# Optimization experiments

Hardware: AMD Instinct MI355X
Metric: run time of the kernel (lower is better)

## Reference

```python
import jax, jax.numpy as jnp
import numpy as np

W_DENSITY, W_COUNT, W_DOMAIN, W_REGIONAL = 100.0, 0.001, 0.5, 1.0
LEVELS = (1, 2, 3)


def setup_inputs() -> dict:
    key = jax.random.key(0)
    k1, k2, k3, k4 = jax.random.split(key, 4)
    B, H, W = 32, 768, 768
    return {
        "pred_density": jax.random.uniform(k1, (B, 1, H, W), dtype=jnp.float32),
        "gt_density": jax.random.uniform(k2, (B, 1, H, W), dtype=jnp.float32),
        "domain_pred_rgb": jax.random.normal(k3, (B, 2), dtype=jnp.float32),
        "domain_pred_thermal": jax.random.normal(k4, (B, 2), dtype=jnp.float32),
    }


def _regional_loss(pred, gt):
    # pred, gt: [B, 1, H, W]; H, W divisible by 2**max(LEVELS)
    B, C, H, W = pred.shape
    total = jnp.float32(0.0)
    last_cells = 1
    for L in LEVELS:
        cells = 2 ** L
        hs, ws = H // cells, W // cells
        # region sums via reshape: [B, C, cells, cells]
        p = pred.reshape(B, C, cells, hs, cells, ws).sum(axis=(3, 5))
        g = gt.reshape(B, C, cells, hs, cells, ws).sum(axis=(3, 5))
        # per-region L1 loss = mean over (B, C), summed over the cells x cells grid
        total = total + jnp.abs(p - g).mean(axis=(0, 1)).sum()
        last_cells = cells
    return total / (len(LEVELS) * last_cells * last_cells)


def _ce_loss(logits, labels):
    # mean over batch of -log_softmax(logits)[label]
    logp = jax.nn.log_softmax(logits, axis=-1)
    return -jnp.take_along_axis(logp, labels[:, None], axis=-1).mean()


def reference(pred_density, gt_density, domain_pred_rgb, domain_pred_thermal):
    B = pred_density.shape[0]
    density_loss = jnp.mean((pred_density - gt_density) ** 2)
    pred_count = pred_density.sum(axis=(2, 3)).squeeze()  # [B]
    gt_count = gt_density.sum(axis=(2, 3)).squeeze()
    count_loss = jnp.abs(pred_count - gt_count).mean()
    regional = _regional_loss(pred_density, gt_density)
    rgb_labels = jnp.zeros((B,), dtype=jnp.int32)
    thermal_labels = jnp.ones((B,), dtype=jnp.int32)
    domain_loss = (_ce_loss(domain_pred_rgb, rgb_labels)
                   + _ce_loss(domain_pred_thermal, thermal_labels)) / 2.0
    total_loss = (W_DENSITY * density_loss + W_COUNT * count_loss
                  + W_REGIONAL * regional + W_DOMAIN * domain_loss)
    return total_loss
```

## Files before the change

### kernel.cpp

```cpp
#include <hip/hip_runtime.h>
#include <math.h>

#define BATCH 32
#define HH 768
#define WW 768
#define RS 96
#define NREG 64
#define NBLK (BATCH * NREG)

__global__ __launch_bounds__(256) void region_reduce(
    const float* __restrict__ pred, const float* __restrict__ gt,
    float* __restrict__ sq_out, float* __restrict__ sp_out,
    float* __restrict__ sg_out)
{
    const int bid = blockIdx.x;
    const int b  = bid >> 6;
    const int r  = bid & 63;
    const int ri = r >> 3, rj = r & 7;
    const size_t base = (size_t)b * (HH * WW) + (size_t)ri * RS * WW + (size_t)rj * RS;
    const float* __restrict__ pb = pred + base;
    const float* __restrict__ gb = gt + base;

    float sp = 0.f, sg = 0.f, sq = 0.f;
    for (int q = threadIdx.x; q < RS * 24; q += 256) {
        const int row = q / 24;
        const int c4  = q - row * 24;
        const float4 p = *(const float4*)(pb + (size_t)row * WW + c4 * 4);
        const float4 g = *(const float4*)(gb + (size_t)row * WW + c4 * 4);
        sp += (p.x + p.y) + (p.z + p.w);
        sg += (g.x + g.y) + (g.z + g.w);
        const float dx = p.x - g.x, dy = p.y - g.y;
        const float dz = p.z - g.z, dw = p.w - g.w;
        sq += (dx * dx + dy * dy) + (dz * dz + dw * dw);
    }

    #pragma unroll
    for (int off = 32; off > 0; off >>= 1) {
        sp += __shfl_down(sp, off, 64);
        sg += __shfl_down(sg, off, 64);
        sq += __shfl_down(sq, off, 64);
    }
    __shared__ float lsp[4], lsg[4], lsq[4];
    const int wave = threadIdx.x >> 6;
    const int lane = threadIdx.x & 63;
    if (lane == 0) { lsp[wave] = sp; lsg[wave] = sg; lsq[wave] = sq; }
    __syncthreads();
    if (threadIdx.x == 0) {
        sp_out[bid] = (lsp[0] + lsp[1]) + (lsp[2] + lsp[3]);
        sg_out[bid] = (lsg[0] + lsg[1]) + (lsg[2] + lsg[3]);
        sq_out[bid] = (lsq[0] + lsq[1]) + (lsq[2] + lsq[3]);
    }
}

__device__ inline float block_sum(float v, float* red, int t) {
    red[t] = v;
    __syncthreads();
    #pragma unroll
    for (int off = 128; off > 0; off >>= 1) {
        if (t < off) red[t] += red[t + off];
        __syncthreads();
    }
    const float r = red[0];
    __syncthreads();
    return r;
}

__global__ __launch_bounds__(256) void finalize(
    const float* __restrict__ sq, const float* __restrict__ sp,
    const float* __restrict__ sg, const float* __restrict__ rgb,
    const float* __restrict__ th, float* __restrict__ out)
{
    __shared__ float d[NBLK];
    __shared__ float d2[BATCH * 16];
    __shared__ float d1[BATCH * 4];
    __shared__ float red[256];
    const int t = threadIdx.x;

    float s_sq = 0.f;
    float l3 = 0.f;
    for (int i = t; i < NBLK; i += 256) {
        s_sq += sq[i];
        const float v = sp[i] - sg[i];
        d[i] = v;
        l3 += fabsf(v);
    }
    __syncthreads();

    float l2 = 0.f;
    for (int i = t; i < BATCH * 16; i += 256) {
        const int b = i >> 4, r2 = i & 15;
        const int i2 = r2 >> 2, j2 = r2 & 3;
        const float* db = d + b * 64;
        const float v = (db[(2 * i2) * 8 + 2 * j2]     + db[(2 * i2) * 8 + 2 * j2 + 1])
                      + (db[(2 * i2 + 1) * 8 + 2 * j2] + db[(2 * i2 + 1) * 8 + 2 * j2 + 1]);
        d2[i] = v;
        l2 += fabsf(v);
    }
    __syncthreads();

    float l1 = 0.f;
    if (t < BATCH * 4) {
        const int b = t >> 2, r1 = t & 3;
        const int i1 = r1 >> 1, j1 = r1 & 1;
        const float* db = d2 + b * 16;
        const float v = (db[(2 * i1) * 4 + 2 * j1]     + db[(2 * i1) * 4 + 2 * j1 + 1])
                      + (db[(2 * i1 + 1) * 4 + 2 * j1] + db[(2 * i1 + 1) * 4 + 2 * j1 + 1]);
        d1[t] = v;
        l1 = fabsf(v);
    }
    __syncthreads();

    float cnt = 0.f, dom = 0.f;
    if (t < BATCH) {
        const float c = (d1[t * 4] + d1[t * 4 + 1]) + (d1[t * 4 + 2] + d1[t * 4 + 3]);
        cnt = fabsf(c);
        const float x0 = rgb[t * 2], x1 = rgb[t * 2 + 1];
        const float mx = fmaxf(x0, x1);
        dom  = (mx + logf(expf(x0 - mx) + expf(x1 - mx))) - x0;
        const float y0 = th[t * 2], y1 = th[t * 2 + 1];
        const float my = fmaxf(y0, y1);
        dom += (my + logf(expf(y0 - my) + expf(y1 - my))) - y1;
    }

    const float S_sq  = block_sum(s_sq, red, t);
    const float S_l3  = block_sum(l3, red, t);
    const float S_l2  = block_sum(l2, red, t);
    const float S_l1  = block_sum(l1, red, t);
    const float S_cnt = block_sum(cnt, red, t);
    const float S_dom = block_sum(dom, red, t);

    if (t == 0) {
        const float density = S_sq / (float)((size_t)BATCH * HH * WW);
        const float count_l = S_cnt / (float)BATCH;
        const float regional = ((S_l1 + S_l2 + S_l3) / (float)BATCH) / 192.0f;
        const float domain = S_dom / 64.0f;
        out[0] = 100.0f * density + 0.001f * count_l + 1.0f * regional
               + 0.5f * domain;
    }
}

extern "C" void kernel_launch(void* const* d_in, const int* in_sizes, int n_in,
                              void* d_out, int out_size, void* d_ws, size_t ws_size,
                              hipStream_t stream) {
    const float* pred = (const float*)d_in[0];
    const float* gt   = (const float*)d_in[1];
    const float* rgb  = (const float*)d_in[2];
    const float* th   = (const float*)d_in[3];
    float* out = (float*)d_out;

    float* sq = (float*)d_ws;
    float* sp = sq + NBLK;
    float* sg = sp + NBLK;

    region_reduce<<<NBLK, 256, 0, stream>>>(pred, gt, sq, sp, sg);
    finalize<<<1, 256, 0, stream>>>(sq, sp, sg, rgb, th, out);
}
```

Baseline: 179.0 us.

## Remap blocks to 12-row strips, batch loads in registers, and use wave-shuffle reductions

Each block now covers a 12-row by 768-column strip instead of a 96x96 region. Each 32-lane group handles one region column, with all 18 float4 loads issued up front into registers to raise memory-level parallelism. Only the per-region partial of pred-gt is written, since that difference is all the L1 terms need, which removes the separate pred and gt sums. The finalize kernel reads these partials with float4 loads and replaces six serial shared-memory tree reductions with wave shuffles. The cost is higher register pressure from 72 live floats per thread and more partial outputs (8 per region) for finalize to combine.

Measured after the change: 171.7 us. -4.1%, faster.

```diff
diff --git a/kernel.cpp b/kernel.cpp
--- a/kernel.cpp
+++ b/kernel.cpp
@@ -4,90 +4,100 @@
 #define BATCH 32
 #define HH 768
 #define WW 768
-#define RS 96
 #define NREG 64
 #define NBLK (BATCH * NREG)
 
 __global__ __launch_bounds__(256) void region_reduce(
     const float* __restrict__ pred, const float* __restrict__ gt,
-    float* __restrict__ sq_out, float* __restrict__ sp_out,
-    float* __restrict__ sg_out)
+    float* __restrict__ sq_out, float* __restrict__ dws)
 {
-    const int bid = blockIdx.x;
-    const int b  = bid >> 6;
-    const int r  = bid & 63;
-    const int ri = r >> 3, rj = r & 7;
-    const size_t base = (size_t)b * (HH * WW) + (size_t)ri * RS * WW + (size_t)rj * RS;
-    const float* __restrict__ pb = pred + base;
-    const float* __restrict__ gb = gt + base;
+    const int bid   = blockIdx.x;
+    const int b     = bid >> 6;
+    const int ri    = (bid >> 3) & 7;
+    const int chunk = bid & 7;
+    const size_t base = (size_t)b * (HH * WW) + (size_t)(ri * 96 + chunk * 12) * WW;
 
-    float sp = 0.f, sg = 0.f, sq = 0.f;
-    for (int q = threadIdx.x; q < RS * 24; q += 256) {
+    const int t = threadIdx.x;
+    const int g = t >> 5;
+    const int l = t & 31;
+
+    const float* __restrict__ pb = pred + base + g * 96;
+    const float* __restrict__ gb = gt   + base + g * 96;
+
+    int offs[9];
+    #pragma unroll
+    for (int k = 0; k < 9; ++k) {
+        const int q   = l + 32 * k;
         const int row = q / 24;
-        const int c4  = q - row * 24;
-        const float4 p = *(const float4*)(pb + (size_t)row * WW + c4 * 4);
-        const float4 g = *(const float4*)(gb + (size_t)row * WW + c4 * 4);
-        sp += (p.x + p.y) + (p.z + p.w);
-        sg += (g.x + g.y) + (g.z + g.w);
-        const float dx = p.x - g.x, dy = p.y - g.y;
-        const float dz = p.z - g.z, dw = p.w - g.w;
+        const int c   = q - row * 24;
+        offs[k] = row * WW + c * 4;
+    }
+    float4 p[9], q4[9];
+    #pragma unroll
+    for (int k = 0; k < 9; ++k) p[k]  = *(const float4*)(pb + offs[k]);
+    #pragma unroll
+    for (int k = 0; k < 9; ++k) q4[k] = *(const float4*)(gb + offs[k]);
+
+    float sq = 0.f, ds = 0.f;
+    #pragma unroll
+    for (int k = 0; k < 9; ++k) {
+        const float dx = p[k].x - q4[k].x;
+        const float dy = p[k].y - q4[k].y;
+        const float dz = p[k].z - q4[k].z;
+        const float dw = p[k].w - q4[k].w;
         sq += (dx * dx + dy * dy) + (dz * dz + dw * dw);
+        ds += (dx + dy) + (dz + dw);
     }
 
     #pragma unroll
-    for (int off = 32; off > 0; off >>= 1) {
-        sp += __shfl_down(sp, off, 64);
-        sg += __shfl_down(sg, off, 64);
-        sq += __shfl_down(sq, off, 64);
-    }
-    __shared__ float lsp[4], lsg[4], lsq[4];
-    const int wave = threadIdx.x >> 6;
-    const int lane = threadIdx.x & 63;
-    if (lane == 0) { lsp[wave] = sp; lsg[wave] = sg; lsq[wave] = sq; }
+    for (int off = 16; off > 0; off >>= 1) ds += __shfl_down(ds, off, 64);
+    #pragma unroll
+    for (int off = 32; off > 0; off >>= 1) sq += __shfl_down(sq, off, 64);
+
+    if (l == 0) dws[((((b << 3) + ri) << 3) + g) * 8 + chunk] = ds;
+
+    __shared__ float lsq[4];
+    const int wave = t >> 6;
+    if ((t & 63) == 0) lsq[wave] = sq;
     __syncthreads();
-    if (threadIdx.x == 0) {
-        sp_out[bid] = (lsp[0] + lsp[1]) + (lsp[2] + lsp[3]);
-        sg_out[bid] = (lsg[0] + lsg[1]) + (lsg[2] + lsg[3]);
-        sq_out[bid] = (lsq[0] + lsq[1]) + (lsq[2] + lsq[3]);
-    }
-}
-
-__device__ inline float block_sum(float v, float* red, int t) {
-    red[t] = v;
-    __syncthreads();
-    #pragma unroll
-    for (int off = 128; off > 0; off >>= 1) {
-        if (t < off) red[t] += red[t + off];
-        __syncthreads();
-    }
-    const float r = red[0];
-    __syncthreads();
-    return r;
+    if (t == 0) sq_out[bid] = (lsq[0] + lsq[1]) + (lsq[2] + lsq[3]);
 }
 
 __global__ __launch_bounds__(256) void finalize(
-    const float* __restrict__ sq, const float* __restrict__ sp,
-    const float* __restrict__ sg, const float* __restrict__ rgb,
-    const float* __restrict__ th, float* __restrict__ out)
+    const float* __restrict__ sq, const float* __restrict__ dws,
+    const float* __restrict__ rgb, const float* __restrict__ th,
+    float* __restrict__ out)
 {
     __shared__ float d[NBLK];
     __shared__ float d2[BATCH * 16];
     __shared__ float d1[BATCH * 4];
-    __shared__ float red[256];
+    __shared__ float redbuf[4 * 6];
     const int t = threadIdx.x;
 
     float s_sq = 0.f;
+    const float4* sq4 = (const float4*)sq;
+    #pragma unroll
+    for (int k = 0; k < 2; ++k) {
+        const float4 v = sq4[t + 256 * k];
+        s_sq += (v.x + v.y) + (v.z + v.w);
+    }
+
     float l3 = 0.f;
-    for (int i = t; i < NBLK; i += 256) {
-        s_sq += sq[i];
-        const float v = sp[i] - sg[i];
-        d[i] = v;
+    #pragma unroll
+    for (int k = 0; k < 8; ++k) {
+        const int r = t + 256 * k;
+        const float4* dp = (const float4*)(dws + r * 8);
+        const float4 a = dp[0], bb = dp[1];
+        const float v = ((a.x + a.y) + (a.z + a.w)) + ((bb.x + bb.y) + (bb.z + bb.w));
+        d[r] = v;
         l3 += fabsf(v);
     }
     __syncthreads();
 
     float l2 = 0.f;
-    for (int i = t; i < BATCH * 16; i += 256) {
+    #pragma unroll
+    for (int k = 0; k < 2; ++k) {
+        const int i = t + 256 * k;
         const int b = i >> 4, r2 = i & 15;
         const int i2 = r2 >> 2, j2 = r2 & 3;
         const float* db = d + b * 64;
@@ -122,20 +132,28 @@
         dom += (my + logf(expf(y0 - my) + expf(y1 - my))) - y1;
     }
 
-    const float S_sq  = block_sum(s_sq, red, t);
-    const float S_l3  = block_sum(l3, red, t);
-    const float S_l2  = block_sum(l2, red, t);
-    const float S_l1  = block_sum(l1, red, t);
-    const float S_cnt = block_sum(cnt, red, t);
-    const float S_dom = block_sum(dom, red, t);
-
+    float vals[6] = {s_sq, l3, l2, l1, cnt, dom};
+    #pragma unroll
+    for (int off = 32; off > 0; off >>= 1) {
+        #pragma unroll
+        for (int j = 0; j < 6; ++j) vals[j] += __shfl_down(vals[j], off, 64);
+    }
+    const int wave = t >> 6;
+    if ((t & 63) == 0) {
+        #pragma unroll
+        for (int j = 0; j < 6; ++j) redbuf[wave * 6 + j] = vals[j];
+    }
+    __syncthreads();
     if (t == 0) {
-        const float density = S_sq / (float)((size_t)BATCH * HH * WW);
-        const float count_l = S_cnt / (float)BATCH;
-        const float regional = ((S_l1 + S_l2 + S_l3) / (float)BATCH) / 192.0f;
-        const float domain = S_dom / 64.0f;
-        out[0] = 100.0f * density + 0.001f * count_l + 1.0f * regional
-               + 0.5f * domain;
+        float S[6];
+        #pragma unroll
+        for (int j = 0; j < 6; ++j)
+            S[j] = (redbuf[j] + redbuf[6 + j]) + (redbuf[12 + j] + redbuf[18 + j]);
+        const float density  = S[0] / (float)((size_t)BATCH * HH * WW);
+        const float count_l  = S[4] / (float)BATCH;
+        const float regional = ((S[3] + S[2] + S[1]) / (float)BATCH) / 192.0f;
+        const float domain   = S[5] / 64.0f;
+        out[0] = 100.0f * density + 0.001f * count_l + 1.0f * regional + 0.5f * domain;
     }
 }
 
@@ -148,10 +166,9 @@
     const float* th   = (const float*)d_in[3];
     float* out = (float*)d_out;
 
-    float* sq = (float*)d_ws;
-    float* sp = sq + NBLK;
-    float* sg = sp + NBLK;
+    float* sq  = (float*)d_ws;
+    float* dws = sq + NBLK;
 
-    region_reduce<<<NBLK, 256, 0, stream>>>(pred, gt, sq, sp, sg);
-    finalize<<<1, 256, 0, stream>>>(sq, sp, sg, rgb, th, out);
+    region_reduce<<<NBLK, 256, 0, stream>>>(pred, gt, sq, dws);
+    finalize<<<1, 256, 0, stream>>>(sq, dws, rgb, th, out);
 }
```
